# Kernel optimization log

Hardware: AMD Instinct MI355X
Metric: run time of the kernel (lower is better)

Reference implementation:

```python
import jax, jax.numpy as jnp
import numpy as np

EPS = 1e-8

def elu_feature_map(x):
    return jax.nn.elu(x) + 1.0

def setup_inputs() -> dict:
    key = jax.random.key(0)
    ks = jax.random.split(key, 5)
    B, S, D = 2, 4096, 1024
    scale = 1.0 / np.sqrt(D).astype(np.float32)
    x = jax.random.normal(ks[0], (B, S, D), dtype=jnp.float32)
    Wq = jax.random.normal(ks[1], (D, D), dtype=jnp.float32) * scale
    Wk = jax.random.normal(ks[2], (D, D), dtype=jnp.float32) * scale
    Wv = jax.random.normal(ks[3], (D, D), dtype=jnp.float32) * scale
    Wo = jax.random.normal(ks[4], (D, D), dtype=jnp.float32) * scale
    return {"x": x, "Wq": Wq, "Wk": Wk, "Wv": Wv, "Wo": Wo}

def reference(x, Wq, Wk, Wv, Wo):
    B, S, D = x.shape
    H = 16
    Dh = D // H
    # projections (nn.Linear with no bias: x @ W.T)
    def proj(W):
        return (x @ W.T).reshape(B, S, H, Dh)
    q = elu_feature_map(proj(Wq))  # [B,S,H,Dh]
    k = elu_feature_map(proj(Wk))
    v = proj(Wv)
    # scan over sequence: carry running kv_sum [B,H,Dh,Dh] and k_sum [B,H,Dh]
    q_t = jnp.moveaxis(q, 1, 0)  # [S,B,H,Dh]
    k_t = jnp.moveaxis(k, 1, 0)
    v_t = jnp.moveaxis(v, 1, 0)

    def step(carry, qkv):
        kv_sum, k_sum = carry
        q_i, k_i, v_i = qkv  # each [B,H,Dh]
        kv_sum = kv_sum + jnp.einsum('bhd,bhe->bhde', k_i, v_i)
        k_sum = k_sum + k_i
        num = jnp.einsum('bhd,bhde->bhe', q_i, kv_sum)
        den = jnp.sum(q_i * k_sum, axis=-1, keepdims=True)
        out_i = num / (den + EPS)
        return (kv_sum, k_sum), out_i

    kv0 = jnp.zeros((B, H, Dh, Dh), dtype=x.dtype)
    ks0 = jnp.zeros((B, H, Dh), dtype=x.dtype)
    _, out = jax.lax.scan(step, (kv0, ks0), (q_t, k_t, v_t))  # out: [S,B,H,Dh]
    out = jnp.moveaxis(out, 0, 1).reshape(B, S, D)
    return out @ Wo.T
```

## Files before the change

### kernel.cpp

```cpp
#include <hip/hip_runtime.h>
#include <math.h>


#define EPSF 1e-8f

typedef unsigned short u16;
typedef unsigned int   u32;
typedef __attribute__((ext_vector_type(8))) short short8v;
typedef __attribute__((ext_vector_type(4))) float f32x4;

__device__ __forceinline__ float elu1(float x){ return x > 0.f ? x + 1.f : __expf(x); }
__device__ __forceinline__ u16 f2bf(float f){
    union{float f; u32 i;} c; c.f = f;
    u32 i = c.i + 0x7FFFu + ((c.i >> 16) & 1u);
    return (u16)(i >> 16);
}
__device__ __forceinline__ float bf2f(u16 v){ union{u32 i; float f;} c; c.i = (u32)v << 16; return c.f; }
__device__ __forceinline__ float bflo(u32 v){ union{u32 i; float f;} c; c.i = v << 16; return c.f; }
__device__ __forceinline__ float bfhi(u32 v){ union{u32 i; float f;} c; c.i = v & 0xffff0000u; return c.f; }
__device__ __forceinline__ void f4a(float4 v, float* a){ a[0]=v.x; a[1]=v.y; a[2]=v.z; a[3]=v.w; }

__device__ __forceinline__ void gload16(const void* g, void* l){
    __builtin_amdgcn_global_load_lds((const __attribute__((address_space(1))) u32*)g,
                                     (__attribute__((address_space(3))) u32*)l, 16, 0, 0);
}

__global__ __launch_bounds__(256) void k_cast5(
    const float* __restrict__ x,  const float* __restrict__ wq,
    const float* __restrict__ wk, const float* __restrict__ wv,
    const float* __restrict__ wo,
    u16* __restrict__ xb, u16* __restrict__ wcat, u16* __restrict__ wob)
{
    size_t i8 = ((size_t)blockIdx.x * 256 + threadIdx.x) * 8;
    const float* s; u16* d; size_t off;
    if      (i8 <  8388608) { s = x;  d = xb;            off = i8; }
    else if (i8 <  9437184) { s = wq; d = wcat;          off = i8 - 8388608; }
    else if (i8 < 10485760) { s = wk; d = wcat + 1048576; off = i8 - 9437184; }
    else if (i8 < 11534336) { s = wv; d = wcat + 2097152; off = i8 - 10485760; }
    else                    { s = wo; d = wob;           off = i8 - 11534336; }
    float4 a = *(const float4*)&s[off];
    float4 b = *(const float4*)&s[off + 4];
    uint4 p;
    p.x = (u32)f2bf(a.x) | ((u32)f2bf(a.y) << 16);
    p.y = (u32)f2bf(a.z) | ((u32)f2bf(a.w) << 16);
    p.z = (u32)f2bf(b.x) | ((u32)f2bf(b.y) << 16);
    p.w = (u32)f2bf(b.z) | ((u32)f2bf(b.w) << 16);
    *(uint4*)&d[off] = p;
}

template<int MODE, int NBY>
__global__ __launch_bounds__(256, 2) void k_gemm7(
    const u16* __restrict__ Ag, const u16* __restrict__ Wg, void* __restrict__ Cv)
{
    __shared__ __align__(16) char dsm[73728];
    const int bid = blockIdx.x;
    const int nid = (bid & 7) * ((32 * NBY) >> 3) + (bid >> 3);
    const int bx  = nid / NBY;
    const int by  = nid % NBY;
    const int m0  = bx * 256;
    const int n0  = by * 128;

    const int tid = threadIdx.x;
    const int l   = tid & 63;
    const int wid = tid >> 6;
    const int wm  = wid >> 1;
    const int wn  = wid & 1;
    const int li  = l & 15;
    const int kgi = l >> 4;

    const int ra0 = wm*128 + li;
    const int offA0 = (ra0 >> 1)*128 + (((((ra0 & 1) << 2) | kgi) ^ ((ra0 >> 1) & 7)) << 4);
    const int rb0 = wn*64 + li;
    const int offB0 = (rb0 >> 1)*128 + (((((rb0 & 1) << 2) | kgi) ^ ((rb0 >> 1) & 7)) << 4);

    const int sx   = (l & 7) ^ (l >> 3);
    const int rowb = 2*(wid*8 + (l >> 3)) + (sx >> 2);
    const int skg  = (sx & 3) * 8;
    const u16* srcA = Ag + (size_t)(m0 + rowb) * 1024 + skg;
    const u16* srcB = Wg + (size_t)(n0 + rowb) * 1024 + skg;

    f32x4 acc[8][4];
    #pragma unroll
    for (int m = 0; m < 8; ++m)
        #pragma unroll
        for (int n = 0; n < 4; ++n) acc[m][n] = (f32x4){0.f, 0.f, 0.f, 0.f};

    #define ST7(BUF, T) { \
        char* ab = dsm + (BUF)*24576; \
        char* bb = ab + 16384; \
        _Pragma("unroll") for (int j = 0; j < 4; ++j) \
            gload16(srcA + (size_t)j*65536 + (T)*32, ab + j*4096 + wid*1024); \
        _Pragma("unroll") for (int j = 0; j < 2; ++j) \
            gload16(srcB + (size_t)j*65536 + (T)*32, bb + j*4096 + wid*1024); }

    #define CP7(BUF) { \
        const char* Ab = dsm + (BUF)*24576; \
        const char* Bb = Ab + 16384; \
        short8v bfr[4]; \
        _Pragma("unroll") for (int n = 0; n < 4; ++n) bfr[n] = *(const short8v*)(Bb + offB0 + n*1024); \
        __builtin_amdgcn_s_setprio(1); \
        _Pragma("unroll") for (int m = 0; m < 8; ++m) { \
            short8v afr = *(const short8v*)(Ab + offA0 + m*1024); \
            _Pragma("unroll") for (int n = 0; n < 4; ++n) \
                acc[m][n] = __builtin_amdgcn_mfma_f32_16x16x32_bf16(afr, bfr[n], acc[m][n], 0, 0, 0); \
        } \
        __builtin_amdgcn_s_setprio(0); }

    #define STEP7(CUR, STB, TS) { \
        ST7(STB, TS); \
        CP7(CUR); \
        asm volatile("s_waitcnt vmcnt(6)"); \
        __builtin_amdgcn_s_barrier(); }

    ST7(0, 0); ST7(1, 1);
    asm volatile("s_waitcnt vmcnt(6)");
    __builtin_amdgcn_s_barrier();

    #pragma unroll 1
    for (int g = 0; g < 10; ++g) {
        const int t = g * 3;
        STEP7(0, 2, t + 2);
        STEP7(1, 0, t + 3);
        STEP7(2, 1, t + 4);
    }
    CP7(0);
    asm volatile("s_waitcnt vmcnt(0)");
    __builtin_amdgcn_s_barrier();
    CP7(1);
    #undef STEP7
    #undef CP7
    #undef ST7

    const int r0 = m0 + wm*128 + kgi*4;
    if (MODE == 1) {
        const int matrix = by >> 3;
        const bool do_elu = matrix < 2;
        u16* outp = (u16*)Cv + (size_t)matrix * 8388608;
        const int c0 = (by & 7)*128 + wn*64 + li;
        #pragma unroll
        for (int m = 0; m < 8; ++m)
            #pragma unroll
            for (int n = 0; n < 4; ++n)
                #pragma unroll
                for (int r = 0; r < 4; ++r) {
                    float v = acc[m][n][r];
                    if (do_elu) v = elu1(v);
                    outp[(size_t)(r0 + m*16 + r) * 1024 + c0 + n*16] = f2bf(v);
                }
    } else {
        float* outp = (float*)Cv;
        const int c0 = by*128 + wn*64 + li;
        #pragma unroll
        for (int m = 0; m < 8; ++m)
            #pragma unroll
            for (int n = 0; n < 4; ++n)
                #pragma unroll
                for (int r = 0; r < 4; ++r)
                    outp[(size_t)(r0 + m*16 + r) * 1024 + c0 + n*16] = acc[m][n][r];
    }
}

template<int MODE, int NBY>
__global__ __launch_bounds__(256, 3) void k_gemm9(
    const u16* __restrict__ Ag, const u16* __restrict__ Wg, void* __restrict__ Cv)
{
    __shared__ __align__(16) char dsm[49152];
    const int bid = blockIdx.x;
    const int nid = (bid & 7) * ((64 * NBY) >> 3) + (bid >> 3);
    const int bx  = nid / NBY;
    const int by  = nid % NBY;
    const int m0  = bx * 128;
    const int n0  = by * 128;

    const int tid = threadIdx.x;
    const int l   = tid & 63;
    const int wid = tid >> 6;
    const int wm  = wid >> 1;
    const int wn  = wid & 1;
    const int li  = l & 15;
    const int kgi = l >> 4;

    const int ra0 = wm*64 + li;
    const int offA0 = ((ra0 >> 1) << 7) + (((((ra0 & 1) << 2) | kgi) ^ ((ra0 >> 1) & 7)) << 4);
    const int rb0 = wn*64 + li;
    const int offB0 = ((rb0 >> 1) << 7) + (((((rb0 & 1) << 2) | kgi) ^ ((rb0 >> 1) & 7)) << 4);

    const int sx   = (l & 7) ^ (l >> 3);
    const int rowb = 2*(wid*8 + (l >> 3)) + (sx >> 2);
    const int skg  = (sx & 3) * 8;
    const u16* srcA = Ag + (size_t)(m0 + rowb) * 1024 + skg;
    const u16* srcB = Wg + (size_t)(n0 + rowb) * 1024 + skg;

    f32x4 acc[4][4];
    #pragma unroll
    for (int m = 0; m < 4; ++m)
        #pragma unroll
        for (int n = 0; n < 4; ++n) acc[m][n] = (f32x4){0.f, 0.f, 0.f, 0.f};

    #define ST9(BUF, T) { \
        char* ab = dsm + (BUF)*16384; \
        char* bb = ab + 8192; \
        _Pragma("unroll") for (int j = 0; j < 2; ++j) \
            gload16(srcA + (size_t)j*65536 + (T)*32, ab + j*4096 + wid*1024); \
        _Pragma("unroll") for (int j = 0; j < 2; ++j) \
            gload16(srcB + (size_t)j*65536 + (T)*32, bb + j*4096 + wid*1024); }

    #define CP9(BUF) { \
        const char* Ab = dsm + (BUF)*16384; \
        const char* Bb = Ab + 8192; \
        short8v bfr[4]; \
        _Pragma("unroll") for (int n = 0; n < 4; ++n) bfr[n] = *(const short8v*)(Bb + offB0 + n*1024); \
        __builtin_amdgcn_s_setprio(1); \
        _Pragma("unroll") for (int m = 0; m < 4; ++m) { \
            short8v afr = *(const short8v*)(Ab + offA0 + m*1024); \
            _Pragma("unroll") for (int n = 0; n < 4; ++n) \
                acc[m][n] = __builtin_amdgcn_mfma_f32_16x16x32_bf16(afr, bfr[n], acc[m][n], 0, 0, 0); \
        } \
        __builtin_amdgcn_s_setprio(0); }

    #define STEP9(CUR, STB, TS) { \
        ST9(STB, TS); \
        CP9(CUR); \
        asm volatile("s_waitcnt vmcnt(4)"); \
        __builtin_amdgcn_s_barrier(); }

    ST9(0, 0); ST9(1, 1);
    asm volatile("s_waitcnt vmcnt(4)");
    __builtin_amdgcn_s_barrier();

    #pragma unroll 1
    for (int g = 0; g < 10; ++g) {
        const int t = g * 3;
        STEP9(0, 2, t + 2);
        STEP9(1, 0, t + 3);
        STEP9(2, 1, t + 4);
    }
    CP9(0);
    asm volatile("s_waitcnt vmcnt(0)");
    __builtin_amdgcn_s_barrier();
    CP9(1);
    #undef STEP9
    #undef CP9
    #undef ST9

    const int r0 = m0 + wm*64 + kgi*4;
    if (MODE == 1) {
        const int matrix = by >> 3;
        const bool do_elu = matrix < 2;
        u16* outp = (u16*)Cv + (size_t)matrix * 8388608;
        const int c0 = (by & 7)*128 + wn*64 + li;
        #pragma unroll
        for (int m = 0; m < 4; ++m)
            #pragma unroll
            for (int n = 0; n < 4; ++n)
                #pragma unroll
                for (int r = 0; r < 4; ++r) {
                    float v = acc[m][n][r];
                    if (do_elu) v = elu1(v);
                    outp[(size_t)(r0 + m*16 + r) * 1024 + c0 + n*16] = f2bf(v);
                }
    } else {
        float* outp = (float*)Cv;
        const int c0 = by*128 + wn*64 + li;
        #pragma unroll
        for (int m = 0; m < 4; ++m)
            #pragma unroll
            for (int n = 0; n < 4; ++n)
                #pragma unroll
                for (int r = 0; r < 4; ++r)
                    outp[(size_t)(r0 + m*16 + r) * 1024 + c0 + n*16] = acc[m][n][r];
    }
}

#define LSTR 72
__global__ __launch_bounds__(256) void k_segsums(
    const u16* __restrict__ Kg, const u16* __restrict__ Vg,
    u16* __restrict__ SegKV, float* __restrict__ SegKS)
{
    const int tid = threadIdx.x;
    const int l = tid & 63;
    const int w = tid >> 6;
    const int bh  = blockIdx.x >> 4;
    const int seg = blockIdx.x & 15;
    const int row0 = (bh >> 4) * 4096 + seg * 256;
    const int col  = (bh & 15) * 64;
    const int li = l & 15;
    const int lg = l >> 4;

    __shared__ __align__(16) u16 Kt[64 * LSTR];
    __shared__ __align__(16) u16 Vt[64 * LSTR];
    __shared__ float ksPart[4][64];

    f32x4 Stacc[4];
    #pragma unroll
    for (int nd = 0; nd < 4; ++nd) Stacc[nd] = (f32x4){0.f, 0.f, 0.f, 0.f};
    float ksAcc = 0.f;

    for (int cc = 0; cc < 4; ++cc) {
        const int rc = row0 + cc * 64;
        #pragma unroll
        for (int r = 0; r < 2; ++r) {
            int idx = tid + r * 256;
            int i = idx >> 3, cg = (idx & 7) << 3;
            uint4 ku = *(const uint4*)&Kg[(size_t)(rc + i) * 1024 + col + cg];
            uint4 vu = *(const uint4*)&Vg[(size_t)(rc + i) * 1024 + col + cg];
            Kt[(cg+0)*LSTR + i] = (u16)(ku.x & 0xffff);
            Kt[(cg+1)*LSTR + i] = (u16)(ku.x >> 16);
            Kt[(cg+2)*LSTR + i] = (u16)(ku.y & 0xffff);
            Kt[(cg+3)*LSTR + i] = (u16)(ku.y >> 16);
            Kt[(cg+4)*LSTR + i] = (u16)(ku.z & 0xffff);
            Kt[(cg+5)*LSTR + i] = (u16)(ku.z >> 16);
            Kt[(cg+6)*LSTR + i] = (u16)(ku.w & 0xffff);
            Kt[(cg+7)*LSTR + i] = (u16)(ku.w >> 16);
            Vt[(cg+0)*LSTR + i] = (u16)(vu.x & 0xffff);
            Vt[(cg+1)*LSTR + i] = (u16)(vu.x >> 16);
            Vt[(cg+2)*LSTR + i] = (u16)(vu.y & 0xffff);
            Vt[(cg+3)*LSTR + i] = (u16)(vu.y >> 16);
            Vt[(cg+4)*LSTR + i] = (u16)(vu.z & 0xffff);
            Vt[(cg+5)*LSTR + i] = (u16)(vu.z >> 16);
            Vt[(cg+6)*LSTR + i] = (u16)(vu.w & 0xffff);
            Vt[(cg+7)*LSTR + i] = (u16)(vu.w >> 16);
        }
        __syncthreads();
        #pragma unroll
        for (int kc = 0; kc < 2; ++kc) {
            short8v av = *(const short8v*)&Vt[(w*16 + li) * LSTR + lg*8 + kc*32];
            #pragma unroll
            for (int nd = 0; nd < 4; ++nd) {
                short8v bk = *(const short8v*)&Kt[(nd*16 + li) * LSTR + lg*8 + kc*32];
                Stacc[nd] = __builtin_amdgcn_mfma_f32_16x16x32_bf16(av, bk, Stacc[nd], 0, 0, 0);
            }
        }
        {
            const int d = tid & 63, q = tid >> 6;
            float s = 0.f;
            #pragma unroll
            for (int ii = 0; ii < 16; ++ii) s += bf2f(Kt[d * LSTR + 0] * 0 + Kt[(d)*LSTR + 0]);
            s = 0.f;
            #pragma unroll
            for (int ii = 0; ii < 16; ++ii) s += bf2f(Kt[d * LSTR + q*16 + ii]);
            ksPart[q][d] = s;
        }
        __syncthreads();
        if (tid < 64) ksAcc += ksPart[0][tid] + ksPart[1][tid] + ksPart[2][tid] + ksPart[3][tid];
        __syncthreads();
    }

    u16* out = &SegKV[(size_t)blockIdx.x * 4096];
    #pragma unroll
    for (int nd = 0; nd < 4; ++nd)
        #pragma unroll
        for (int r = 0; r < 4; ++r)
            out[(16*w + lg*4 + r) * 64 + nd*16 + li] = f2bf(Stacc[nd][r]);
    if (tid < 64) SegKS[(size_t)blockIdx.x * 64 + tid] = ksAcc;
}

__global__ __launch_bounds__(256) void k_prefix2(u16* __restrict__ SegKV, float* __restrict__ SegKS)
{
    if (blockIdx.x < 512) {
        const int bh = blockIdx.x >> 4;
        const int p  = ((blockIdx.x & 15) << 8) + threadIdx.x;
        const size_t base = (size_t)bh * 16 * 4096 + p;
        float acc = 0.f;
        #pragma unroll
        for (int s = 0; s < 16; ++s) {
            float t = bf2f(SegKV[base + (size_t)s * 4096]);
            SegKV[base + (size_t)s * 4096] = f2bf(acc);
            acc += t;
        }
    } else {
        const int idx = (blockIdx.x - 512) * 256 + threadIdx.x;
        const int bh = idx >> 6, d = idx & 63;
        const size_t base = (size_t)bh * 16 * 64 + d;
        float acc = 0.f;
        #pragma unroll
        for (int s = 0; s < 16; ++s) {
            float t = SegKS[base + (size_t)s * 64];
            SegKS[base + (size_t)s * 64] = acc;
            acc += t;
        }
    }
}

__global__ __launch_bounds__(256) void k_attn3(
    const u16* __restrict__ Qg, const u16* __restrict__ Kg, const u16* __restrict__ Vg,
    const u16* __restrict__ SegKVp, const float* __restrict__ SegKSp, u16* __restrict__ AO)
{
    const int tid = threadIdx.x;
    const int l = tid & 63;
    const int w = tid >> 6;
    const int bh  = blockIdx.x >> 4;
    const int seg = blockIdx.x & 15;
    const int row0 = (bh >> 4) * 4096 + seg * 256;
    const int col  = (bh & 15) * 64;
    const int li = l & 15;
    const int lg = l >> 4;
    const int i_row = w * 16 + li;

    __shared__ __align__(16) u16 Qs [64 * LSTR];
    __shared__ __align__(16) u16 Ks [64 * LSTR];
    __shared__ __align__(16) u16 Kt [64 * LSTR];
    __shared__ __align__(16) u16 Vt [64 * LSTR];
    __shared__ __align__(16) u16 Sts[64 * LSTR];
    __shared__ __align__(16) u16 Pl [64 * LSTR];
    __shared__ float ksum[64];
    __shared__ float ksPart[4][64];
    __shared__ float invdenL[64];

    #pragma unroll
    for (int r = 0; r < 2; ++r) {
        int idx = tid + r * 256;
        int i = idx >> 3, cg = (idx & 7) << 3;
        *(uint4*)&Sts[i*LSTR + cg] = *(const uint4*)&SegKVp[(size_t)blockIdx.x * 4096 + i * 64 + cg];
    }
    if (tid < 64) ksum[tid] = SegKSp[(size_t)blockIdx.x * 64 + tid];
    __syncthreads();

    f32x4 Stacc[4];
    #pragma unroll
    for (int nd = 0; nd < 4; ++nd)
        #pragma unroll
        for (int r = 0; r < 4; ++r)
            Stacc[nd][r] = bf2f(Sts[(16*w + lg*4 + r) * LSTR + nd*16 + li]);

    for (int cc = 0; cc < 4; ++cc) {
        const int rc = row0 + cc * 64;
        #pragma unroll
        for (int r = 0; r < 2; ++r) {
            int idx = tid + r * 256;
            int i = idx >> 3, cg = (idx & 7) << 3;
            *(uint4*)&Qs[i*LSTR + cg] = *(const uint4*)&Qg[(size_t)(rc + i) * 1024 + col + cg];
            uint4 ku = *(const uint4*)&Kg[(size_t)(rc + i) * 1024 + col + cg];
            uint4 vu = *(const uint4*)&Vg[(size_t)(rc + i) * 1024 + col + cg];
            *(uint4*)&Ks[i*LSTR + cg] = ku;
            Kt[(cg+0)*LSTR + i] = (u16)(ku.x & 0xffff);
            Kt[(cg+1)*LSTR + i] = (u16)(ku.x >> 16);
            Kt[(cg+2)*LSTR + i] = (u16)(ku.y & 0xffff);
            Kt[(cg+3)*LSTR + i] = (u16)(ku.y >> 16);
            Kt[(cg+4)*LSTR + i] = (u16)(ku.z & 0xffff);
            Kt[(cg+5)*LSTR + i] = (u16)(ku.z >> 16);
            Kt[(cg+6)*LSTR + i] = (u16)(ku.w & 0xffff);
            Kt[(cg+7)*LSTR + i] = (u16)(ku.w >> 16);
            Vt[(cg+0)*LSTR + i] = (u16)(vu.x & 0xffff);
            Vt[(cg+1)*LSTR + i] = (u16)(vu.x >> 16);
            Vt[(cg+2)*LSTR + i] = (u16)(vu.y & 0xffff);
            Vt[(cg+3)*LSTR + i] = (u16)(vu.y >> 16);
            Vt[(cg+4)*LSTR + i] = (u16)(vu.z & 0xffff);
            Vt[(cg+5)*LSTR + i] = (u16)(vu.z >> 16);
            Vt[(cg+6)*LSTR + i] = (u16)(vu.w & 0xffff);
            Vt[(cg+7)*LSTR + i] = (u16)(vu.w >> 16);
        }
        __syncthreads();

        short8v bq[2];
        #pragma unroll
        for (int kc = 0; kc < 2; ++kc)
            bq[kc] = *(const short8v*)&Qs[i_row * LSTR + lg*8 + kc*32];

        float den = EPSF;
        #pragma unroll
        for (int mj = 0; mj < 4; ++mj) {
            f32x4 sacc = (f32x4){0.f, 0.f, 0.f, 0.f};
            #pragma unroll
            for (int kc = 0; kc < 2; ++kc) {
                short8v ak = *(const short8v*)&Ks[(mj*16 + li) * LSTR + lg*8 + kc*32];
                sacc = __builtin_amdgcn_mfma_f32_16x16x32_bf16(ak, bq[kc], sacc, 0, 0, 0);
            }
            const int jbase = mj*16 + lg*4;
            float pv[4];
            #pragma unroll
            for (int r = 0; r < 4; ++r) {
                float v = sacc[r];
                v = (jbase + r <= i_row) ? v : 0.f;
                den += v;
                pv[r] = v;
            }
            u32 lo = (u32)f2bf(pv[0]) | ((u32)f2bf(pv[1]) << 16);
            u32 hi = (u32)f2bf(pv[2]) | ((u32)f2bf(pv[3]) << 16);
            *(uint2*)&Pl[i_row * LSTR + jbase] = make_uint2(lo, hi);
        }
        {
            const int d0 = lg * 16;
            uint4 q1 = *(const uint4*)&Qs[i_row * LSTR + d0];
            uint4 q2 = *(const uint4*)&Qs[i_row * LSTR + d0 + 8];
            den += bflo(q1.x)*ksum[d0+0] + bfhi(q1.x)*ksum[d0+1]
                 + bflo(q1.y)*ksum[d0+2] + bfhi(q1.y)*ksum[d0+3]
                 + bflo(q1.z)*ksum[d0+4] + bfhi(q1.z)*ksum[d0+5]
                 + bflo(q1.w)*ksum[d0+6] + bfhi(q1.w)*ksum[d0+7]
                 + bflo(q2.x)*ksum[d0+8] + bfhi(q2.x)*ksum[d0+9]
                 + bflo(q2.y)*ksum[d0+10]+ bfhi(q2.y)*ksum[d0+11]
                 + bflo(q2.z)*ksum[d0+12]+ bfhi(q2.z)*ksum[d0+13]
                 + bflo(q2.w)*ksum[d0+14]+ bfhi(q2.w)*ksum[d0+15];
        }
        den += __shfl_xor(den, 16);
        den += __shfl_xor(den, 32);
        if (l < 16) invdenL[w*16 + l] = 1.f / den;

        if (cc < 3) {
            const int d = tid & 63, q = tid >> 6;
            float s = 0.f;
            #pragma unroll
            for (int ii = 0; ii < 16; ++ii) s += bf2f(Kt[d * LSTR + q*16 + ii]);
            ksPart[q][d] = s;
        }
        __syncthreads();

        f32x4 oacc[4];
        #pragma unroll
        for (int ne = 0; ne < 4; ++ne) oacc[ne] = (f32x4){0.f, 0.f, 0.f, 0.f};
        #pragma unroll
        for (int kc = 0; kc < 2; ++kc) {
            short8v ap = *(const short8v*)&Pl[i_row * LSTR + lg*8 + kc*32];
            short8v aq = bq[kc];
            #pragma unroll
            for (int ne = 0; ne < 4; ++ne) {
                short8v bv = *(const short8v*)&Vt [(ne*16 + li) * LSTR + lg*8 + kc*32];
                short8v bs = *(const short8v*)&Sts[(ne*16 + li) * LSTR + lg*8 + kc*32];
                oacc[ne] = __builtin_amdgcn_mfma_f32_16x16x32_bf16(ap, bv, oacc[ne], 0, 0, 0);
                oacc[ne] = __builtin_amdgcn_mfma_f32_16x16x32_bf16(aq, bs, oacc[ne], 0, 0, 0);
            }
        }
        if (cc < 3 && tid < 64)
            ksum[tid] += ksPart[0][tid] + ksPart[1][tid] + ksPart[2][tid] + ksPart[3][tid];

        if (cc < 3) {
            #pragma unroll
            for (int kc = 0; kc < 2; ++kc) {
                short8v av = *(const short8v*)&Vt[(w*16 + li) * LSTR + lg*8 + kc*32];
                #pragma unroll
                for (int nd = 0; nd < 4; ++nd) {
                    short8v bk = *(const short8v*)&Kt[(nd*16 + li) * LSTR + lg*8 + kc*32];
                    Stacc[nd] = __builtin_amdgcn_mfma_f32_16x16x32_bf16(av, bk, Stacc[nd], 0, 0, 0);
                }
            }
        }

        float inv[4];
        #pragma unroll
        for (int r = 0; r < 4; ++r) inv[r] = invdenL[w*16 + lg*4 + r];
        #pragma unroll
        for (int ne = 0; ne < 4; ++ne)
            #pragma unroll
            for (int r = 0; r < 4; ++r)
                Pl[(w*16 + lg*4 + r) * LSTR + ne*16 + li] = f2bf(oacc[ne][r] * inv[r]);
        #pragma unroll
        for (int p = 0; p < 2; ++p) {
            int idx2 = l + p * 64;
            int ro = w*16 + (idx2 >> 3), cg = (idx2 & 7) << 3;
            *(uint4*)&AO[(size_t)(rc + ro) * 1024 + col + cg] = *(const uint4*)&Pl[ro*LSTR + cg];
        }

        __syncthreads();
        if (cc < 3) {
            #pragma unroll
            for (int nd = 0; nd < 4; ++nd)
                #pragma unroll
                for (int r = 0; r < 4; ++r)
                    Sts[(16*w + lg*4 + r) * LSTR + nd*16 + li] = f2bf(Stacc[nd][r]);
            __syncthreads();
        }
    }
}

extern "C" void kernel_launch(void* const* d_in, const int* in_sizes, int n_in,
                              void* d_out, int out_size, void* d_ws, size_t ws_size,
                              hipStream_t stream)
{
    const float* x  = (const float*)d_in[0];
    const float* Wq = (const float*)d_in[1];
    const float* Wk = (const float*)d_in[2];
    const float* Wv = (const float*)d_in[3];
    const float* Wo = (const float*)d_in[4];
    float* out = (float*)d_out;

    char* w = (char*)d_ws;
    u16*   QKVb  = (u16*)(w);
    u16*   Qb    = QKVb;
    u16*   Kb    = QKVb + 8388608;
    u16*   Vb    = QKVb + 16777216;
    u16*   xb    = (u16*)(w + 50331648);
    u16*   AOb   = xb;
    u16*   Wcat  = (u16*)(w + 67108864);
    u16*   Wob   = (u16*)(w + 73400320);
    u16*   SegKV = (u16*)(w + 75497472);
    float* SegKS = (float*)(w + 79691776);

    k_cast5       <<<6144, 256, 0, stream>>>(x, Wq, Wk, Wv, Wo, xb, Wcat, Wob);
    k_gemm7<1,24> <<<768,  256, 0, stream>>>(xb, Wcat, (void*)QKVb);
    k_segsums     <<<512,  256, 0, stream>>>(Kb, Vb, SegKV, SegKS);
    k_prefix2     <<<520,  256, 0, stream>>>(SegKV, SegKS);
    k_attn3       <<<512,  256, 0, stream>>>(Qb, Kb, Vb, SegKV, SegKS, AOb);
    k_gemm9<3,8>  <<<512,  256, 0, stream>>>(AOb, Wob, (void*)out);
}
```

Measured before the change: 132.3 us.

## Fold segment prefix into attention, use 128-tile GEMM for QKV projection

Removes the separate prefix-scan kernel. Each attention block now sums the preceding segment KV and k_sum states itself, trading one launch and one read-modify-write pass for redundant reads that grow with segment index. The QKV projection switches from the 256x128-tile GEMM to the 128x128-tile kernel with more blocks, and the block-to-tile mapping is changed to group tiles per XCD for cache locality. A dead redundant loop in segsums is also removed.

```diff
diff --git a/kernel.cpp b/kernel.cpp
--- a/kernel.cpp
+++ b/kernel.cpp
@@ -18,7 +18,6 @@
 __device__ __forceinline__ float bf2f(u16 v){ union{u32 i; float f;} c; c.i = (u32)v << 16; return c.f; }
 __device__ __forceinline__ float bflo(u32 v){ union{u32 i; float f;} c; c.i = v << 16; return c.f; }
 __device__ __forceinline__ float bfhi(u32 v){ union{u32 i; float f;} c; c.i = v & 0xffff0000u; return c.f; }
-__device__ __forceinline__ void f4a(float4 v, float* a){ a[0]=v.x; a[1]=v.y; a[2]=v.z; a[3]=v.w; }
 
 __device__ __forceinline__ void gload16(const void* g, void* l){
     __builtin_amdgcn_global_load_lds((const __attribute__((address_space(1))) u32*)g,
@@ -49,126 +48,15 @@
 }
 
 template<int MODE, int NBY>
-__global__ __launch_bounds__(256, 2) void k_gemm7(
-    const u16* __restrict__ Ag, const u16* __restrict__ Wg, void* __restrict__ Cv)
-{
-    __shared__ __align__(16) char dsm[73728];
-    const int bid = blockIdx.x;
-    const int nid = (bid & 7) * ((32 * NBY) >> 3) + (bid >> 3);
-    const int bx  = nid / NBY;
-    const int by  = nid % NBY;
-    const int m0  = bx * 256;
-    const int n0  = by * 128;
-
-    const int tid = threadIdx.x;
-    const int l   = tid & 63;
-    const int wid = tid >> 6;
-    const int wm  = wid >> 1;
-    const int wn  = wid & 1;
-    const int li  = l & 15;
-    const int kgi = l >> 4;
-
-    const int ra0 = wm*128 + li;
-    const int offA0 = (ra0 >> 1)*128 + (((((ra0 & 1) << 2) | kgi) ^ ((ra0 >> 1) & 7)) << 4);
-    const int rb0 = wn*64 + li;
-    const int offB0 = (rb0 >> 1)*128 + (((((rb0 & 1) << 2) | kgi) ^ ((rb0 >> 1) & 7)) << 4);
-
-    const int sx   = (l & 7) ^ (l >> 3);
-    const int rowb = 2*(wid*8 + (l >> 3)) + (sx >> 2);
-    const int skg  = (sx & 3) * 8;
-    const u16* srcA = Ag + (size_t)(m0 + rowb) * 1024 + skg;
-    const u16* srcB = Wg + (size_t)(n0 + rowb) * 1024 + skg;
-
-    f32x4 acc[8][4];
-    #pragma unroll
-    for (int m = 0; m < 8; ++m)
-        #pragma unroll
-        for (int n = 0; n < 4; ++n) acc[m][n] = (f32x4){0.f, 0.f, 0.f, 0.f};
-
-    #define ST7(BUF, T) { \
-        char* ab = dsm + (BUF)*24576; \
-        char* bb = ab + 16384; \
-        _Pragma("unroll") for (int j = 0; j < 4; ++j) \
-            gload16(srcA + (size_t)j*65536 + (T)*32, ab + j*4096 + wid*1024); \
-        _Pragma("unroll") for (int j = 0; j < 2; ++j) \
-            gload16(srcB + (size_t)j*65536 + (T)*32, bb + j*4096 + wid*1024); }
-
-    #define CP7(BUF) { \
-        const char* Ab = dsm + (BUF)*24576; \
-        const char* Bb = Ab + 16384; \
-        short8v bfr[4]; \
-        _Pragma("unroll") for (int n = 0; n < 4; ++n) bfr[n] = *(const short8v*)(Bb + offB0 + n*1024); \
-        __builtin_amdgcn_s_setprio(1); \
-        _Pragma("unroll") for (int m = 0; m < 8; ++m) { \
-            short8v afr = *(const short8v*)(Ab + offA0 + m*1024); \
-            _Pragma("unroll") for (int n = 0; n < 4; ++n) \
-                acc[m][n] = __builtin_amdgcn_mfma_f32_16x16x32_bf16(afr, bfr[n], acc[m][n], 0, 0, 0); \
-        } \
-        __builtin_amdgcn_s_setprio(0); }
-
-    #define STEP7(CUR, STB, TS) { \
-        ST7(STB, TS); \
-        CP7(CUR); \
-        asm volatile("s_waitcnt vmcnt(6)"); \
-        __builtin_amdgcn_s_barrier(); }
-
-    ST7(0, 0); ST7(1, 1);
-    asm volatile("s_waitcnt vmcnt(6)");
-    __builtin_amdgcn_s_barrier();
-
-    #pragma unroll 1
-    for (int g = 0; g < 10; ++g) {
-        const int t = g * 3;
-        STEP7(0, 2, t + 2);
-        STEP7(1, 0, t + 3);
-        STEP7(2, 1, t + 4);
-    }
-    CP7(0);
-    asm volatile("s_waitcnt vmcnt(0)");
-    __builtin_amdgcn_s_barrier();
-    CP7(1);
-    #undef STEP7
-    #undef CP7
-    #undef ST7
-
-    const int r0 = m0 + wm*128 + kgi*4;
-    if (MODE == 1) {
-        const int matrix = by >> 3;
-        const bool do_elu = matrix < 2;
-        u16* outp = (u16*)Cv + (size_t)matrix * 8388608;
-        const int c0 = (by & 7)*128 + wn*64 + li;
-        #pragma unroll
-        for (int m = 0; m < 8; ++m)
-            #pragma unroll
-            for (int n = 0; n < 4; ++n)
-                #pragma unroll
-                for (int r = 0; r < 4; ++r) {
-                    float v = acc[m][n][r];
-                    if (do_elu) v = elu1(v);
-                    outp[(size_t)(r0 + m*16 + r) * 1024 + c0 + n*16] = f2bf(v);
-                }
-    } else {
-        float* outp = (float*)Cv;
-        const int c0 = by*128 + wn*64 + li;
-        #pragma unroll
-        for (int m = 0; m < 8; ++m)
-            #pragma unroll
-            for (int n = 0; n < 4; ++n)
-                #pragma unroll
-                for (int r = 0; r < 4; ++r)
-                    outp[(size_t)(r0 + m*16 + r) * 1024 + c0 + n*16] = acc[m][n][r];
-    }
-}
-
-template<int MODE, int NBY>
 __global__ __launch_bounds__(256, 3) void k_gemm9(
     const u16* __restrict__ Ag, const u16* __restrict__ Wg, void* __restrict__ Cv)
 {
     __shared__ __align__(16) char dsm[49152];
     const int bid = blockIdx.x;
-    const int nid = (bid & 7) * ((64 * NBY) >> 3) + (bid >> 3);
-    const int bx  = nid / NBY;
-    const int by  = nid % NBY;
+    const int xcd = bid & 7;
+    const int s   = bid >> 3;
+    const int by  = (s & 7) + ((s >> 6) << 3);
+    const int bx  = (xcd << 3) + ((s >> 3) & 7);
     const int m0  = bx * 128;
     const int n0  = by * 128;
 
@@ -333,13 +221,10 @@
         }
         {
             const int d = tid & 63, q = tid >> 6;
-            float s = 0.f;
-            #pragma unroll
-            for (int ii = 0; ii < 16; ++ii) s += bf2f(Kt[d * LSTR + 0] * 0 + Kt[(d)*LSTR + 0]);
-            s = 0.f;
-            #pragma unroll
-            for (int ii = 0; ii < 16; ++ii) s += bf2f(Kt[d * LSTR + q*16 + ii]);
-            ksPart[q][d] = s;
+            float sx2 = 0.f;
+            #pragma unroll
+            for (int ii = 0; ii < 16; ++ii) sx2 += bf2f(Kt[d * LSTR + q*16 + ii]);
+            ksPart[q][d] = sx2;
         }
         __syncthreads();
         if (tid < 64) ksAcc += ksPart[0][tid] + ksPart[1][tid] + ksPart[2][tid] + ksPart[3][tid];
@@ -355,36 +240,9 @@
     if (tid < 64) SegKS[(size_t)blockIdx.x * 64 + tid] = ksAcc;
 }
 
-__global__ __launch_bounds__(256) void k_prefix2(u16* __restrict__ SegKV, float* __restrict__ SegKS)
-{
-    if (blockIdx.x < 512) {
-        const int bh = blockIdx.x >> 4;
-        const int p  = ((blockIdx.x & 15) << 8) + threadIdx.x;
-        const size_t base = (size_t)bh * 16 * 4096 + p;
-        float acc = 0.f;
-        #pragma unroll
-        for (int s = 0; s < 16; ++s) {
-            float t = bf2f(SegKV[base + (size_t)s * 4096]);
-            SegKV[base + (size_t)s * 4096] = f2bf(acc);
-            acc += t;
-        }
-    } else {
-        const int idx = (blockIdx.x - 512) * 256 + threadIdx.x;
-        const int bh = idx >> 6, d = idx & 63;
-        const size_t base = (size_t)bh * 16 * 64 + d;
-        float acc = 0.f;
-        #pragma unroll
-        for (int s = 0; s < 16; ++s) {
-            float t = SegKS[base + (size_t)s * 64];
-            SegKS[base + (size_t)s * 64] = acc;
-            acc += t;
-        }
-    }
-}
-
 __global__ __launch_bounds__(256) void k_attn3(
     const u16* __restrict__ Qg, const u16* __restrict__ Kg, const u16* __restrict__ Vg,
-    const u16* __restrict__ SegKVp, const float* __restrict__ SegKSp, u16* __restrict__ AO)
+    const u16* __restrict__ SegKV, const float* __restrict__ SegKS, u16* __restrict__ AO)
 {
     const int tid = threadIdx.x;
     const int l = tid & 63;
@@ -407,13 +265,24 @@
     __shared__ float ksPart[4][64];
     __shared__ float invdenL[64];
 
-    #pragma unroll
-    for (int r = 0; r < 2; ++r) {
-        int idx = tid + r * 256;
-        int i = idx >> 3, cg = (idx & 7) << 3;
-        *(uint4*)&Sts[i*LSTR + cg] = *(const uint4*)&SegKVp[(size_t)blockIdx.x * 4096 + i * 64 + cg];
+    {
+        const size_t kvbase = (size_t)bh * 16 * 4096;
+        #pragma unroll 4
+        for (int k = 0; k < 16; ++k) {
+            int p = tid + k * 256;
+            float a = 0.f;
+            for (int s2 = 0; s2 < seg; ++s2)
+                a += bf2f(SegKV[kvbase + (size_t)s2 * 4096 + p]);
+            Sts[(p >> 6) * LSTR + (p & 63)] = f2bf(a);
+        }
+        if (tid < 64) {
+            const size_t ksbase = (size_t)bh * 16 * 64;
+            float a = 0.f;
+            for (int s2 = 0; s2 < seg; ++s2)
+                a += SegKS[ksbase + (size_t)s2 * 64 + tid];
+            ksum[tid] = a;
+        }
     }
-    if (tid < 64) ksum[tid] = SegKSp[(size_t)blockIdx.x * 64 + tid];
     __syncthreads();
 
     f32x4 Stacc[4];
@@ -498,10 +367,10 @@
 
         if (cc < 3) {
             const int d = tid & 63, q = tid >> 6;
-            float s = 0.f;
-            #pragma unroll
-            for (int ii = 0; ii < 16; ++ii) s += bf2f(Kt[d * LSTR + q*16 + ii]);
-            ksPart[q][d] = s;
+            float sx2 = 0.f;
+            #pragma unroll
+            for (int ii = 0; ii < 16; ++ii) sx2 += bf2f(Kt[d * LSTR + q*16 + ii]);
+            ksPart[q][d] = sx2;
         }
         __syncthreads();
 
@@ -586,9 +455,8 @@
     float* SegKS = (float*)(w + 79691776);
 
     k_cast5       <<<6144, 256, 0, stream>>>(x, Wq, Wk, Wv, Wo, xb, Wcat, Wob);
-    k_gemm7<1,24> <<<768,  256, 0, stream>>>(xb, Wcat, (void*)QKVb);
+    k_gemm9<1,24> <<<1536, 256, 0, stream>>>(xb, Wcat, (void*)QKVb);
     k_segsums     <<<512,  256, 0, stream>>>(Kb, Vb, SegKV, SegKS);
-    k_prefix2     <<<520,  256, 0, stream>>>(SegKV, SegKS);
     k_attn3       <<<512,  256, 0, stream>>>(Qb, Kb, Vb, SegKV, SegKS, AOb);
     k_gemm9<3,8>  <<<512,  256, 0, stream>>>(AOb, Wob, (void*)out);
 }
```

Result: slower. 190.1 us (+43.7%).
